# Kernel optimization log

Measured on AMD Instinct MI355X. Metric: run time of the kernel, lower is better.

## Reference

```python
import jax, jax.numpy as jnp
import numpy as np

BN_EPS = 1e-5

def setup_inputs() -> dict:
    key = jax.random.key(0)
    ks = jax.random.split(key, 16)
    B, n, m, C1, C2 = 16, 4096, 1024, 128, 256
    Cin, H1, H2 = C1 + C2, 256, 128  # mlp = [384, 256, 128]
    inp = {
        "unknown": jax.random.normal(ks[0], (B, n, 3), jnp.float32),
        "known": jax.random.normal(ks[1], (B, m, 3), jnp.float32),
        "unknow_feats": jax.random.normal(ks[2], (B, n, C1), jnp.float32),
        "known_feats": jax.random.normal(ks[3], (B, m, C2), jnp.float32),
        # layer 1: 1x1 conv (Cin->H1) + BN (eval stats) + ReLU
        "W1": jax.random.normal(ks[4], (H1, Cin), jnp.float32) * 0.05,
        "b1": jnp.zeros((H1,), jnp.float32),
        "g1": jnp.ones((H1,), jnp.float32),
        "bt1": jnp.zeros((H1,), jnp.float32),
        "mu1": jax.random.normal(ks[5], (H1,), jnp.float32) * 0.1,
        "v1": jax.random.uniform(ks[6], (H1,), jnp.float32, 0.5, 1.5),
        # layer 2: 1x1 conv (H1->H2) + BN + ReLU
        "W2": jax.random.normal(ks[7], (H2, H1), jnp.float32) * 0.05,
        "b2": jnp.zeros((H2,), jnp.float32),
        "g2": jnp.ones((H2,), jnp.float32),
        "bt2": jnp.zeros((H2,), jnp.float32),
        "mu2": jax.random.normal(ks[8], (H2,), jnp.float32) * 0.1,
        "v2": jax.random.uniform(ks[9], (H2,), jnp.float32, 0.5, 1.5),
    }
    return inp

def _fp_forward(unknown, known, unknow_feats, known_feats,
                W1, b1, g1, bt1, mu1, v1,
                W2, b2, g2, bt2, mu2, v2):
    # --- three_nn: brute-force k=3 nearest neighbors (squared distances) ---
    # d2: (B, n, m)
    d2 = jnp.sum((unknown[:, :, None, :] - known[:, None, :, :]) ** 2, axis=-1)
    neg_dist, idx = jax.lax.top_k(-d2, 3)          # (B, n, 3)
    dist = -neg_dist + 1e-10
    dist_recip = 1.0 / dist
    weight = dist_recip / jnp.sum(dist_recip, axis=2, keepdims=True)  # (B, n, 3)
    # --- three_interpolate: inverse-distance weighted gather ---
    feats_nn = jax.vmap(lambda f, i: f[i])(known_feats, idx)  # (B, n, 3, C2)
    interpolated = jnp.einsum('bnkc,bnk->bnc', feats_nn, weight)
    x = jnp.concatenate([interpolated, unknow_feats], axis=-1)  # (B, n, C1+C2)
    # --- SharedMLP: 1x1 conv + BN(eval) + ReLU, twice ---
    for (W, b, g, bt, mu, v) in ((W1, b1, g1, bt1, mu1, v1),
                                 (W2, b2, g2, bt2, mu2, v2)):
        x = jnp.einsum('bnc,oc->bno', x, W) + b
        x = (x - mu) * (g * jax.lax.rsqrt(v + BN_EPS)) + bt
        x = jax.nn.relu(x)
    return x  # (B, n, mlp[-1])

def reference(unknown, known, unknow_feats, known_feats,
              W1, b1, g1, bt1, mu1, v1,
              W2, b2, g2, bt2, mu2, v2):
    return _fp_forward(unknown, known, unknow_feats, known_feats,
                       W1, b1, g1, bt1, mu1, v1,
                       W2, b2, g2, bt2, mu2, v2)
```

## Files before the change

### kernel.cpp

```cpp
#include <hip/hip_runtime.h>
#include <stdint.h>

typedef float f32x4 __attribute__((ext_vector_type(4)));
typedef __bf16 bf16x8 __attribute__((ext_vector_type(8)));

#define BN_EPS 1e-5f

__device__ __forceinline__ unsigned short f2bf(float x) {
  union { float f; unsigned u; } v; v.f = x;
  unsigned r = v.u + 0x7fffu + ((v.u >> 16) & 1u);
  return (unsigned short)(r >> 16);
}

__global__ void prep_kernel(const float* __restrict__ W1, const float* __restrict__ b1,
                            const float* __restrict__ g1, const float* __restrict__ bt1,
                            const float* __restrict__ mu1, const float* __restrict__ v1,
                            const float* __restrict__ W2, const float* __restrict__ b2,
                            const float* __restrict__ g2, const float* __restrict__ bt2,
                            const float* __restrict__ mu2, const float* __restrict__ v2,
                            unsigned short* __restrict__ W1b, unsigned short* __restrict__ W2b,
                            float* __restrict__ bias1, float* __restrict__ bias2) {
  int tid = blockIdx.x * 256 + threadIdx.x;
  if (tid < 98304) {
    int o = tid / 384;
    float s = g1[o] * rsqrtf(v1[o] + BN_EPS);
    W1b[tid] = f2bf(W1[tid] * s);
    if (tid < 256) bias1[tid] = (b1[tid] - mu1[tid]) * (g1[tid] * rsqrtf(v1[tid] + BN_EPS)) + bt1[tid];
  } else if (tid < 98304 + 32768) {
    int t = tid - 98304;
    int o = t / 256;
    float s = g2[o] * rsqrtf(v2[o] + BN_EPS);
    W2b[t] = f2bf(W2[t] * s);
    if (t < 128) bias2[t] = (b2[t] - mu2[t]) * (g2[t] * rsqrtf(v2[t] + BN_EPS)) + bt2[t];
  }
}

__global__ __launch_bounds__(512, 4)
void fp_fused_kernel(const float* __restrict__ unknown, const float* __restrict__ known,
                     const float* __restrict__ unknow_feats, const float* __restrict__ known_feats,
                     const unsigned short* __restrict__ W1b, const unsigned short* __restrict__ W2b,
                     const float* __restrict__ bias1, const float* __restrict__ bias2,
                     float* __restrict__ out) {
  __shared__ __align__(16) unsigned char smem[49152];
  __shared__ float w_s[192];
  __shared__ int   i_s[192];

  float* sd          = (float*)smem;
  unsigned short* si = (unsigned short*)(smem + 12544);
  float4* kxyz       = (float4*)(smem + 18816);
  unsigned char* xA  = smem;
  unsigned char* xB  = smem + 32768;

  int bid = blockIdx.x;
  int swz = ((bid & 7) << 7) | (bid >> 3);
  int b   = swz >> 6;
  int i0  = (swz & 63) << 6;
  int tid = threadIdx.x;

  {
    float* kf = (float*)kxyz;
    for (int t = tid; t < 3072; t += 512) {
      int r = t / 3, c = t - r * 3;
      kf[r * 4 + c] = known[b * 3072 + t];
    }
  }
  int u  = tid & 31;
  int qc = tid >> 5;
  const float* up = unknown + ((size_t)b * 4096 + i0 + 2 * u) * 3;
  float ax = up[0], ay = up[1], az = up[2];
  float bx = up[3], by = up[4], bz = up[5];
  __syncthreads();

  {
    float a0 = 3e38f, a1 = 3e38f, a2 = 3e38f;
    float e0 = 3e38f, e1 = 3e38f, e2 = 3e38f;
    int aj0 = 0, aj1 = 0, aj2 = 0, ej0 = 0, ej1 = 0, ej2 = 0;
    int jb = qc << 6;
    #pragma unroll 4
    for (int jj = 0; jj < 64; ++jj) {
      int j = jb + jj;
      float4 k = kxyz[j];
      {
        float dx = ax - k.x, dy = ay - k.y, dz = az - k.z;
        float d = dx * dx + dy * dy + dz * dz;
        bool c0 = d < a0, c1 = d < a1, c2 = d < a2;
        aj2 = c1 ? aj1 : (c2 ? j : aj2);
        aj1 = c0 ? aj0 : (c1 ? j : aj1);
        aj0 = c0 ? j : aj0;
        float na2 = __builtin_amdgcn_fmed3f(a1, a2, d);
        float na1 = __builtin_amdgcn_fmed3f(a0, a1, d);
        a0 = fminf(a0, d); a1 = na1; a2 = na2;
      }
      {
        float dx = bx - k.x, dy = by - k.y, dz = bz - k.z;
        float d = dx * dx + dy * dy + dz * dz;
        bool c0 = d < e0, c1 = d < e1, c2 = d < e2;
        ej2 = c1 ? ej1 : (c2 ? j : ej2);
        ej1 = c0 ? ej0 : (c1 ? j : ej1);
        ej0 = c0 ? j : ej0;
        float na2 = __builtin_amdgcn_fmed3f(e1, e2, d);
        float na1 = __builtin_amdgcn_fmed3f(e0, e1, d);
        e0 = fminf(e0, d); e1 = na1; e2 = na2;
      }
    }
    int base = (2 * u) * 49 + qc * 3;
    sd[base] = a0; sd[base + 1] = a1; sd[base + 2] = a2;
    si[base] = (unsigned short)aj0; si[base + 1] = (unsigned short)aj1; si[base + 2] = (unsigned short)aj2;
    base += 49;
    sd[base] = e0; sd[base + 1] = e1; sd[base + 2] = e2;
    si[base] = (unsigned short)ej0; si[base + 1] = (unsigned short)ej1; si[base + 2] = (unsigned short)ej2;
  }
  __syncthreads();

  if (tid < 64) {
    float m0 = 3e38f, m1 = 3e38f, m2 = 3e38f;
    int n0 = 0, n1 = 0, n2 = 0;
    int base = tid * 49;
    for (int e = 0; e < 48; ++e) {
      float d = sd[base + e]; int j = si[base + e];
      bool c0 = d < m0, c1 = d < m1, c2 = d < m2;
      n2 = c1 ? n1 : (c2 ? j : n2);
      n1 = c0 ? n0 : (c1 ? j : n1);
      n0 = c0 ? j : n0;
      float t2 = __builtin_amdgcn_fmed3f(m1, m2, d);
      float t1 = __builtin_amdgcn_fmed3f(m0, m1, d);
      m0 = fminf(m0, d); m1 = t1; m2 = t2;
    }
    float r0 = 1.0f / (m0 + 1e-10f);
    float r1 = 1.0f / (m1 + 1e-10f);
    float r2 = 1.0f / (m2 + 1e-10f);
    float rs = 1.0f / (r0 + r1 + r2);
    w_s[tid * 3 + 0] = r0 * rs; i_s[tid * 3 + 0] = n0;
    w_s[tid * 3 + 1] = r1 * rs; i_s[tid * 3 + 1] = n1;
    w_s[tid * 3 + 2] = r2 * rs; i_s[tid * 3 + 2] = n2;
  } else {
    int t0 = tid - 64;
    const float4* uf = (const float4*)(unknow_feats + ((size_t)b * 4096 + i0) * 128);
    for (int t = t0; t < 2048; t += 448) {
      int p  = t >> 5;
      int cq = t & 31;
      float4 v = uf[p * 32 + cq];
      ushort4 h;
      h.x = f2bf(v.x); h.y = f2bf(v.y); h.z = f2bf(v.z); h.w = f2bf(v.w);
      int byte = p * 256 + cq * 8;
      byte ^= (p & 7) << 4;
      *(ushort4*)(xB + byte) = h;
    }
  }
  __syncthreads();

  {
    int pp = tid >> 6;
    int cq = tid & 63;
    const float4* kf = (const float4*)(known_feats + (size_t)b * 1024 * 256);
    #pragma unroll 2
    for (int po = 0; po < 8; ++po) {
      int p = po * 8 + pp;
      int ia = i_s[p * 3 + 0], ib = i_s[p * 3 + 1], ic = i_s[p * 3 + 2];
      float wa = w_s[p * 3 + 0], wb = w_s[p * 3 + 1], wc = w_s[p * 3 + 2];
      float4 va = kf[ia * 64 + cq];
      float4 vb = kf[ib * 64 + cq];
      float4 vc = kf[ic * 64 + cq];
      ushort4 h;
      h.x = f2bf(wa * va.x + wb * vb.x + wc * vc.x);
      h.y = f2bf(wa * va.y + wb * vb.y + wc * vc.y);
      h.z = f2bf(wa * va.z + wb * vb.z + wc * vc.z);
      h.w = f2bf(wa * va.w + wb * vb.w + wc * vc.w);
      int byte = p * 512 + cq * 8;
      byte ^= (p & 7) << 4;
      *(ushort4*)(xA + byte) = h;
    }
  }
  __syncthreads();

  int l  = tid & 63;
  int q  = tid >> 6;
  int lr = l & 15;
  int lk = l >> 4;
  f32x4 acc[4][2];
  #pragma unroll
  for (int m = 0; m < 4; ++m)
    #pragma unroll
    for (int n = 0; n < 2; ++n) acc[m][n] = (f32x4){0.f, 0.f, 0.f, 0.f};

  __builtin_amdgcn_s_setprio(1);
  #pragma unroll
  for (int kk = 0; kk < 12; ++kk) {
    int kb = kk * 32 + lk * 8;
    bf16x8 a[4];
    #pragma unroll
    for (int m = 0; m < 4; ++m) {
      int row = m * 16 + lr;
      if (kk < 8) {
        int byte = row * 512 + kb * 2;
        byte ^= (row & 7) << 4;
        a[m] = *(const bf16x8*)(xA + byte);
      } else {
        int byte = row * 256 + (kb - 256) * 2;
        byte ^= (row & 7) << 4;
        a[m] = *(const bf16x8*)(xB + byte);
      }
    }
    #pragma unroll
    for (int n = 0; n < 2; ++n) {
      int wr = q * 32 + n * 16 + lr;
      bf16x8 bb = *(const bf16x8*)(W1b + wr * 384 + kb);
      #pragma unroll
      for (int m = 0; m < 4; ++m)
        acc[m][n] = __builtin_amdgcn_mfma_f32_16x16x32_bf16(a[m], bb, acc[m][n], 0, 0, 0);
    }
  }
  __builtin_amdgcn_s_setprio(0);

  float bs1[2];
  #pragma unroll
  for (int n = 0; n < 2; ++n) bs1[n] = bias1[q * 32 + n * 16 + lr];

  __syncthreads();
  #pragma unroll
  for (int m = 0; m < 4; ++m)
    #pragma unroll
    for (int n = 0; n < 2; ++n)
      #pragma unroll
      for (int i = 0; i < 4; ++i) {
        int r = m * 16 + lk * 4 + i;
        int c = q * 32 + n * 16 + lr;
        float val = fmaxf(acc[m][n][i] + bs1[n], 0.0f);
        int byte = r * 512 + c * 2;
        byte ^= (r & 7) << 4;
        *(unsigned short*)(xA + byte) = f2bf(val);
      }
  __syncthreads();

  f32x4 acc2[4];
  #pragma unroll
  for (int m = 0; m < 4; ++m) acc2[m] = (f32x4){0.f, 0.f, 0.f, 0.f};

  __builtin_amdgcn_s_setprio(1);
  #pragma unroll
  for (int kk = 0; kk < 8; ++kk) {
    int kb = kk * 32 + lk * 8;
    bf16x8 a[4];
    #pragma unroll
    for (int m = 0; m < 4; ++m) {
      int row = m * 16 + lr;
      int byte = row * 512 + kb * 2;
      byte ^= (row & 7) << 4;
      a[m] = *(const bf16x8*)(xA + byte);
    }
    int wr = q * 16 + lr;
    bf16x8 bb = *(const bf16x8*)(W2b + wr * 256 + kb);
    #pragma unroll
    for (int m = 0; m < 4; ++m)
      acc2[m] = __builtin_amdgcn_mfma_f32_16x16x32_bf16(a[m], bb, acc2[m], 0, 0, 0);
  }
  __builtin_amdgcn_s_setprio(0);

  float bs2 = bias2[q * 16 + lr];

  __syncthreads();
  float* ot = (float*)smem;
  #pragma unroll
  for (int m = 0; m < 4; ++m)
    #pragma unroll
    for (int i = 0; i < 4; ++i) {
      int r = m * 16 + lk * 4 + i;
      int c = q * 16 + lr;
      ot[r * 132 + c] = fmaxf(acc2[m][i] + bs2, 0.0f);
    }
  __syncthreads();
  {
    float4* out4 = (float4*)(out + ((size_t)b * 4096 + i0) * 128);
    #pragma unroll
    for (int t = tid; t < 2048; t += 512) {
      int pr = t >> 5;
      int c4 = t & 31;
      float4 v = *(const float4*)(ot + pr * 132 + c4 * 4);
      out4[pr * 32 + c4] = v;
    }
  }
}

extern "C" void kernel_launch(void* const* d_in, const int* in_sizes, int n_in,
                              void* d_out, int out_size, void* d_ws, size_t ws_size,
                              hipStream_t stream) {
  const float* unknown      = (const float*)d_in[0];
  const float* known        = (const float*)d_in[1];
  const float* unknow_feats = (const float*)d_in[2];
  const float* known_feats  = (const float*)d_in[3];
  const float* W1  = (const float*)d_in[4];
  const float* b1  = (const float*)d_in[5];
  const float* g1  = (const float*)d_in[6];
  const float* bt1 = (const float*)d_in[7];
  const float* mu1 = (const float*)d_in[8];
  const float* v1  = (const float*)d_in[9];
  const float* W2  = (const float*)d_in[10];
  const float* b2  = (const float*)d_in[11];
  const float* g2  = (const float*)d_in[12];
  const float* bt2 = (const float*)d_in[13];
  const float* mu2 = (const float*)d_in[14];
  const float* v2  = (const float*)d_in[15];

  unsigned short* W1b = (unsigned short*)d_ws;
  unsigned short* W2b = W1b + 98304;
  float* bias1 = (float*)(W2b + 32768);
  float* bias2 = bias1 + 256;

  prep_kernel<<<512, 256, 0, stream>>>(W1, b1, g1, bt1, mu1, v1,
                                       W2, b2, g2, bt2, mu2, v2,
                                       W1b, W2b, bias1, bias2);
  fp_fused_kernel<<<1024, 512, 0, stream>>>(unknown, known, unknow_feats, known_feats,
                                            W1b, W2b, bias1, bias2, (float*)d_out);
}
```

Measured before the change: 74.66 us.

## Split fused kernel into separate three-NN and MLP kernels

Splits the single fused kernel into a three-nearest-neighbour kernel and an interpolation-plus-MLP kernel. They communicate through a global buffer of weights and packed 10-bit indices. The NN kernel uses less shared memory and a higher occupancy bound, and the MLP kernel now loads unknow_feats with all threads. The cost is an extra launch and a global round trip for the neighbour data, and the NN and MLP phases no longer overlap inside one block.

```diff
diff --git a/kernel.cpp b/kernel.cpp
--- a/kernel.cpp
+++ b/kernel.cpp
@@ -35,21 +35,13 @@
   }
 }
 
-__global__ __launch_bounds__(512, 4)
-void fp_fused_kernel(const float* __restrict__ unknown, const float* __restrict__ known,
-                     const float* __restrict__ unknow_feats, const float* __restrict__ known_feats,
-                     const unsigned short* __restrict__ W1b, const unsigned short* __restrict__ W2b,
-                     const float* __restrict__ bias1, const float* __restrict__ bias2,
-                     float* __restrict__ out) {
-  __shared__ __align__(16) unsigned char smem[49152];
-  __shared__ float w_s[192];
-  __shared__ int   i_s[192];
-
+__global__ __launch_bounds__(512, 8)
+void nn3_kernel(const float* __restrict__ unknown, const float* __restrict__ known,
+                float4* __restrict__ wi4) {
+  __shared__ __align__(16) unsigned char smem[35200];
   float* sd          = (float*)smem;
   unsigned short* si = (unsigned short*)(smem + 12544);
   float4* kxyz       = (float4*)(smem + 18816);
-  unsigned char* xA  = smem;
-  unsigned char* xB  = smem + 32768;
 
   int bid = blockIdx.x;
   int swz = ((bid & 7) << 7) | (bid >> 3);
@@ -130,13 +122,45 @@
     float r1 = 1.0f / (m1 + 1e-10f);
     float r2 = 1.0f / (m2 + 1e-10f);
     float rs = 1.0f / (r0 + r1 + r2);
-    w_s[tid * 3 + 0] = r0 * rs; i_s[tid * 3 + 0] = n0;
-    w_s[tid * 3 + 1] = r1 * rs; i_s[tid * 3 + 1] = n1;
-    w_s[tid * 3 + 2] = r2 * rs; i_s[tid * 3 + 2] = n2;
-  } else {
-    int t0 = tid - 64;
+    float4 o;
+    o.x = r0 * rs; o.y = r1 * rs; o.z = r2 * rs;
+    o.w = __int_as_float(n0 | (n1 << 10) | (n2 << 20));
+    wi4[(size_t)b * 4096 + i0 + tid] = o;
+  }
+}
+
+__global__ __launch_bounds__(512, 4)
+void mlp_kernel(const float4* __restrict__ wi4,
+                const float* __restrict__ unknow_feats, const float* __restrict__ known_feats,
+                const unsigned short* __restrict__ W1b, const unsigned short* __restrict__ W2b,
+                const float* __restrict__ bias1, const float* __restrict__ bias2,
+                float* __restrict__ out) {
+  __shared__ __align__(16) unsigned char smem[49152];
+  __shared__ float w_s[192];
+  __shared__ int   i_s[192];
+
+  unsigned char* xA = smem;
+  unsigned char* xB = smem + 32768;
+
+  int bid = blockIdx.x;
+  int swz = ((bid & 7) << 7) | (bid >> 3);
+  int b   = swz >> 6;
+  int i0  = (swz & 63) << 6;
+  int tid = threadIdx.x;
+
+  if (tid < 64) {
+    float4 v = wi4[(size_t)b * 4096 + i0 + tid];
+    w_s[tid * 3 + 0] = v.x; w_s[tid * 3 + 1] = v.y; w_s[tid * 3 + 2] = v.z;
+    int pk = __float_as_int(v.w);
+    i_s[tid * 3 + 0] = pk & 1023;
+    i_s[tid * 3 + 1] = (pk >> 10) & 1023;
+    i_s[tid * 3 + 2] = (pk >> 20) & 1023;
+  }
+  {
     const float4* uf = (const float4*)(unknow_feats + ((size_t)b * 4096 + i0) * 128);
-    for (int t = t0; t < 2048; t += 448) {
+    #pragma unroll
+    for (int po = 0; po < 4; ++po) {
+      int t = po * 512 + tid;
       int p  = t >> 5;
       int cq = t & 31;
       float4 v = uf[p * 32 + cq];
@@ -305,10 +329,12 @@
   unsigned short* W2b = W1b + 98304;
   float* bias1 = (float*)(W2b + 32768);
   float* bias2 = bias1 + 256;
+  float4* wi4  = (float4*)((char*)d_ws + 263680);
 
   prep_kernel<<<512, 256, 0, stream>>>(W1, b1, g1, bt1, mu1, v1,
                                        W2, b2, g2, bt2, mu2, v2,
                                        W1b, W2b, bias1, bias2);
-  fp_fused_kernel<<<1024, 512, 0, stream>>>(unknown, known, unknow_feats, known_feats,
-                                            W1b, W2b, bias1, bias2, (float*)d_out);
-}
+  nn3_kernel<<<1024, 512, 0, stream>>>(unknown, known, wi4);
+  mlp_kernel<<<1024, 512, 0, stream>>>(wi4, unknow_feats, known_feats,
+                                       W1b, W2b, bias1, bias2, (float*)d_out);
+}
```

After: 90.72 us. 1.22x slower.

## Reuse one LDS buffer for interpolated and unknown features to shrink shared memory

Applied to the files above, without the earlier changes.

Drops the separate 16KB LDS buffer for unknow_feats and time-multiplexes the single 32KB xA buffer instead. The first half of the interpolated channels is consumed by MFMA first. That region is then overwritten with bf16 unknow_feats while the second half of the interpolated channels is consumed. The aim is to cut LDS per block so more blocks fit on a CU. In exchange, the unknow_feats load no longer overlaps the kNN stage done by warp 0, and the GEMM is split into three phases with extra barriers.

```diff
diff --git a/kernel.cpp b/kernel.cpp
--- a/kernel.cpp
+++ b/kernel.cpp
@@ -41,7 +41,7 @@
                      const unsigned short* __restrict__ W1b, const unsigned short* __restrict__ W2b,
                      const float* __restrict__ bias1, const float* __restrict__ bias2,
                      float* __restrict__ out) {
-  __shared__ __align__(16) unsigned char smem[49152];
+  __shared__ __align__(16) unsigned char smem[35200];
   __shared__ float w_s[192];
   __shared__ int   i_s[192];
 
@@ -49,7 +49,6 @@
   unsigned short* si = (unsigned short*)(smem + 12544);
   float4* kxyz       = (float4*)(smem + 18816);
   unsigned char* xA  = smem;
-  unsigned char* xB  = smem + 32768;
 
   int bid = blockIdx.x;
   int swz = ((bid & 7) << 7) | (bid >> 3);
@@ -133,73 +132,115 @@
     w_s[tid * 3 + 0] = r0 * rs; i_s[tid * 3 + 0] = n0;
     w_s[tid * 3 + 1] = r1 * rs; i_s[tid * 3 + 1] = n1;
     w_s[tid * 3 + 2] = r2 * rs; i_s[tid * 3 + 2] = n2;
-  } else {
-    int t0 = tid - 64;
+  }
+  __syncthreads();
+
+  int l = tid & 63;
+  int q = tid >> 6;
+  {
+    const float4* kf = (const float4*)(known_feats + (size_t)b * 1024 * 256);
+    #pragma unroll 2
+    for (int po = 0; po < 8; ++po) {
+      int p = po * 8 + q;
+      int ia = i_s[p * 3 + 0], ib = i_s[p * 3 + 1], ic = i_s[p * 3 + 2];
+      float wa = w_s[p * 3 + 0], wb = w_s[p * 3 + 1], wc = w_s[p * 3 + 2];
+      float4 va = kf[ia * 64 + l];
+      float4 vb = kf[ib * 64 + l];
+      float4 vc = kf[ic * 64 + l];
+      ushort4 h;
+      h.x = f2bf(wa * va.x + wb * vb.x + wc * vc.x);
+      h.y = f2bf(wa * va.y + wb * vb.y + wc * vc.y);
+      h.z = f2bf(wa * va.z + wb * vb.z + wc * vc.z);
+      h.w = f2bf(wa * va.w + wb * vb.w + wc * vc.w);
+      int byte = p * 512 + l * 8;
+      byte ^= (p & 7) << 4;
+      *(ushort4*)(xA + byte) = h;
+    }
+  }
+  __syncthreads();
+
+  int lr = l & 15;
+  int lk = l >> 4;
+  f32x4 acc[4][2];
+  #pragma unroll
+  for (int m = 0; m < 4; ++m)
+    #pragma unroll
+    for (int n = 0; n < 2; ++n) acc[m][n] = (f32x4){0.f, 0.f, 0.f, 0.f};
+
+  __builtin_amdgcn_s_setprio(1);
+  #pragma unroll
+  for (int kk = 0; kk < 4; ++kk) {
+    int kb = kk * 32 + lk * 8;
+    bf16x8 a[4];
+    #pragma unroll
+    for (int m = 0; m < 4; ++m) {
+      int row = m * 16 + lr;
+      int byte = row * 512 + kb * 2;
+      byte ^= (row & 7) << 4;
+      a[m] = *(const bf16x8*)(xA + byte);
+    }
+    #pragma unroll
+    for (int n = 0; n < 2; ++n) {
+      int wr = q * 32 + n * 16 + lr;
+      bf16x8 bb = *(const bf16x8*)(W1b + wr * 384 + kb);
+      #pragma unroll
+      for (int m = 0; m < 4; ++m)
+        acc[m][n] = __builtin_amdgcn_mfma_f32_16x16x32_bf16(a[m], bb, acc[m][n], 0, 0, 0);
+    }
+  }
+  __builtin_amdgcn_s_setprio(0);
+  __syncthreads();
+
+  {
     const float4* uf = (const float4*)(unknow_feats + ((size_t)b * 4096 + i0) * 128);
-    for (int t = t0; t < 2048; t += 448) {
+    #pragma unroll
+    for (int po = 0; po < 4; ++po) {
+      int t = po * 512 + tid;
       int p  = t >> 5;
       int cq = t & 31;
       float4 v = uf[p * 32 + cq];
       ushort4 h;
       h.x = f2bf(v.x); h.y = f2bf(v.y); h.z = f2bf(v.z); h.w = f2bf(v.w);
-      int byte = p * 256 + cq * 8;
-      byte ^= (p & 7) << 4;
-      *(ushort4*)(xB + byte) = h;
-    }
-  }
-  __syncthreads();
-
-  {
-    int pp = tid >> 6;
-    int cq = tid & 63;
-    const float4* kf = (const float4*)(known_feats + (size_t)b * 1024 * 256);
-    #pragma unroll 2
-    for (int po = 0; po < 8; ++po) {
-      int p = po * 8 + pp;
-      int ia = i_s[p * 3 + 0], ib = i_s[p * 3 + 1], ic = i_s[p * 3 + 2];
-      float wa = w_s[p * 3 + 0], wb = w_s[p * 3 + 1], wc = w_s[p * 3 + 2];
-      float4 va = kf[ia * 64 + cq];
-      float4 vb = kf[ib * 64 + cq];
-      float4 vc = kf[ic * 64 + cq];
-      ushort4 h;
-      h.x = f2bf(wa * va.x + wb * vb.x + wc * vc.x);
-      h.y = f2bf(wa * va.y + wb * vb.y + wc * vc.y);
-      h.z = f2bf(wa * va.z + wb * vb.z + wc * vc.z);
-      h.w = f2bf(wa * va.w + wb * vb.w + wc * vc.w);
       int byte = p * 512 + cq * 8;
       byte ^= (p & 7) << 4;
       *(ushort4*)(xA + byte) = h;
     }
   }
-  __syncthreads();
-
-  int l  = tid & 63;
-  int q  = tid >> 6;
-  int lr = l & 15;
-  int lk = l >> 4;
-  f32x4 acc[4][2];
-  #pragma unroll
-  for (int m = 0; m < 4; ++m)
-    #pragma unroll
-    for (int n = 0; n < 2; ++n) acc[m][n] = (f32x4){0.f, 0.f, 0.f, 0.f};
-
   __builtin_amdgcn_s_setprio(1);
   #pragma unroll
-  for (int kk = 0; kk < 12; ++kk) {
+  for (int kk = 4; kk < 8; ++kk) {
     int kb = kk * 32 + lk * 8;
     bf16x8 a[4];
     #pragma unroll
     for (int m = 0; m < 4; ++m) {
       int row = m * 16 + lr;
-      if (kk < 8) {
-        int byte = row * 512 + kb * 2;
-        byte ^= (row & 7) << 4;
-        a[m] = *(const bf16x8*)(xA + byte);
-      } else {
-        int byte = row * 256 + (kb - 256) * 2;
-        byte ^= (row & 7) << 4;
-        a[m] = *(const bf16x8*)(xB + byte);
-      }
+      int byte = row * 512 + kb * 2;
+      byte ^= (row & 7) << 4;
+      a[m] = *(const bf16x8*)(xA + byte);
+    }
+    #pragma unroll
+    for (int n = 0; n < 2; ++n) {
+      int wr = q * 32 + n * 16 + lr;
+      bf16x8 bb = *(const bf16x8*)(W1b + wr * 384 + kb);
+      #pragma unroll
+      for (int m = 0; m < 4; ++m)
+        acc[m][n] = __builtin_amdgcn_mfma_f32_16x16x32_bf16(a[m], bb, acc[m][n], 0, 0, 0);
+    }
+  }
+  __builtin_amdgcn_s_setprio(0);
+  __syncthreads();
+
+  __builtin_amdgcn_s_setprio(1);
+  #pragma unroll
+  for (int kk = 8; kk < 12; ++kk) {
+    int kb = kk * 32 + lk * 8;
+    bf16x8 a[4];
+    #pragma unroll
+    for (int m = 0; m < 4; ++m) {
+      int row = m * 16 + lr;
+      int byte = row * 512 + (kb - 256) * 2;
+      byte ^= (row & 7) << 4;
+      a[m] = *(const bf16x8*)(xA + byte);
     }
     #pragma unroll
     for (int n = 0; n < 2; ++n) {
```

Result: slower. 78.18 us (+4.7%).
